# Kernel tuning notes

Measured on AMD Instinct MI355X. Metric: run time of the kernel, lower is better.

## Reference

```python
import jax, jax.numpy as jnp
import numpy as np

# NOTE: the original source omits the definitions of QSVT, quantum_lcu_block,
# QuantumSumBlock and KANLayer. We reconstruct the standard math these blocks
# implement in quantum-KAN papers/repos:
#   QSVT(x)            -> vector of Chebyshev polynomials T_1..T_D of the
#                         (squashed) input, the polynomial basis QSVT realizes.
#   quantum_lcu_block  -> linear combination of unitaries: weighted sum of the
#                         QSVT vector normalized by the LCU l1 weight norm.
#   QuantumSumBlock    -> learnable interference sum: mean_k sin(alpha_k * v).
#   KANLayer           -> Chebyshev-KAN layer: spline term (Chebyshev basis
#                         contracted with coeffs) + SiLU base branch + bias.
# Everything is fully vectorized over (B, F) instead of the original per-scalar
# Python loops.

B, F, DEG, C, KBASIS = 16384, 512, 8, 10, 8


def _cheb(x, K):
    """Chebyshev features T_1..T_K of x in (-1, 1): shape x.shape + (K,)."""
    t = jnp.arccos(jnp.clip(x, -1.0, 1.0))
    k = jnp.arange(1, K + 1, dtype=x.dtype)
    return jnp.cos(t[..., None] * k)


def setup_inputs() -> dict:
    key = jax.random.key(0)
    ks = jax.random.split(key, 6)
    return {
        "X": jax.random.normal(ks[0], (B, F), dtype=jnp.float32),
        # nn.Parameter(torch.rand(num_features, degree))
        "lcu_weights": jax.random.uniform(ks[1], (F, DEG), dtype=jnp.float32),
        # one QuantumSumBlock(degree) per feature -> (F, DEG) phases
        "sum_alpha": jax.random.normal(ks[2], (F, DEG), dtype=jnp.float32),
        # KANLayer params
        "kan_coeff": jax.random.normal(ks[3], (C, F, KBASIS), dtype=jnp.float32) * 0.1,
        "kan_base": jax.random.normal(ks[4], (C, F), dtype=jnp.float32) * 0.1,
        "kan_bias": jnp.zeros((C,), dtype=jnp.float32),
    }


def reference(X, lcu_weights, sum_alpha, kan_coeff, kan_base, kan_bias):
    # squash inputs into the open interval (-1, 1) for the Chebyshev/QSVT basis
    x = 0.99 * jnp.tanh(X)                                   # (B, F)
    # QSVT polynomial feature vector per scalar, batched: (B, F, DEG)
    qsvt = _cheb(x, lcu_weights.shape[1])
    # LCU block: weighted combination normalized by l1 norm of weights -> (B, F)
    lcu = jnp.einsum('bfd,fd->bf', qsvt, lcu_weights) / (
        jnp.sum(jnp.abs(lcu_weights), axis=-1) + 1e-8)
    # Quantum sum block: learnable sinusoidal interference sum -> (B, F)
    summed = jnp.mean(jnp.sin(lcu[..., None] * sum_alpha), axis=-1)
    # Chebyshev-KAN layer
    s = 0.99 * jnp.tanh(summed)
    phi = _cheb(s, kan_coeff.shape[2])                       # (B, F, KBASIS)
    logits = (jnp.einsum('bfk,cfk->bc', phi, kan_coeff)
              + jax.nn.silu(summed) @ kan_base.T
              + kan_bias)                                    # (B, C)
    return logits
```

## Files before the change

### kernel.cpp

```cpp
#include <hip/hip_runtime.h>
#include <hip/hip_bf16.h>

#define BATCH 16384
#define NF    512
#define DEG   8
#define NC    10
#define KB    8

#define RB    16
#define PITCH (NF + 4)
#define NT    256

#define CBN (NC * NF * KB)
#define BBN (NC * NF)

#define INV2PI 0.15915494309189535f
#define LOG2E  1.4426950408889634f

typedef __attribute__((ext_vector_type(2))) float v2f;
typedef __attribute__((ext_vector_type(8))) short bfrag;
typedef __attribute__((ext_vector_type(4))) float f32x4;

union frag_u { bfrag s; unsigned u[4]; };

__device__ unsigned short g_pk[CBN + BBN];

__device__ __forceinline__ v2f v2fma(v2f a, v2f b, v2f c) {
    return __builtin_elementwise_fma(a, b, c);
}
__device__ __forceinline__ v2f v2exp2(v2f a) {
    v2f r; r.x = __builtin_amdgcn_exp2f(a.x); r.y = __builtin_amdgcn_exp2f(a.y);
    return r;
}
__device__ __forceinline__ v2f v2rcp(v2f x) {
    v2f r; r.x = __builtin_amdgcn_rcpf(x.x); r.y = __builtin_amdgcn_rcpf(x.y);
    return r;
}
__device__ __forceinline__ v2f v2sin2pi(v2f x) {
    v2f r; r.x = __builtin_amdgcn_sinf(x.x); r.y = __builtin_amdgcn_sinf(x.y);
    return r;
}
__device__ __forceinline__ v2f v2tanh99(v2f x) {
    v2f e = v2exp2(x * (2.0f * LOG2E));
    v2f r = v2rcp(e + 1.0f);
    return v2fma(r, (v2f)(-1.98f), (v2f)(0.99f));
}
__device__ __forceinline__ v2f v2silu(v2f v) {
    v2f e = v2exp2(v * (-LOG2E));
    v2f r = v2rcp(e + 1.0f);
    return v * r;
}
__device__ __forceinline__ unsigned cvtpk2(float lo, float hi) {
    __hip_bfloat162 h = __float22bfloat162_rn(float2{lo, hi});
    unsigned u;
    __builtin_memcpy(&u, &h, sizeof(u));
    return u;
}

__global__ __launch_bounds__(256) void prep_kernel(
    const float* __restrict__ coeff, const float* __restrict__ base)
{
    const int i = blockIdx.x * 256 + threadIdx.x;
    if (i < CBN)
        g_pk[i] = (unsigned short)((__builtin_bit_cast(unsigned, coeff[i]) + 0x8000u) >> 16);
    else if (i < CBN + BBN)
        g_pk[i] = (unsigned short)((__builtin_bit_cast(unsigned, base[i - CBN]) + 0x8000u) >> 16);
}

__global__ __launch_bounds__(NT, 4) void qkan_kernel(
    const float* __restrict__ X,
    const float* __restrict__ lcu_w,
    const float* __restrict__ alpha,
    const float* __restrict__ bias,
    float* __restrict__ out)
{
    __shared__ float s_mem[RB * PITCH];
    __shared__ float s_red[4 * RB * 16];

    const int t    = threadIdx.x;
    const int row0 = blockIdx.x * RB;

    {
        const int fA = t * 2;

        float wa[2][DEG], aa[2][DEG], den[2];
#pragma unroll
        for (int i = 0; i < 2; ++i) {
            const float4 w0 = *(const float4*)(lcu_w + (fA + i) * DEG);
            const float4 w1 = *(const float4*)(lcu_w + (fA + i) * DEG + 4);
            const float4 a0 = *(const float4*)(alpha + (fA + i) * DEG);
            const float4 a1 = *(const float4*)(alpha + (fA + i) * DEG + 4);
            wa[i][0]=w0.x; wa[i][1]=w0.y; wa[i][2]=w0.z; wa[i][3]=w0.w;
            wa[i][4]=w1.x; wa[i][5]=w1.y; wa[i][6]=w1.z; wa[i][7]=w1.w;
            aa[i][0]=a0.x; aa[i][1]=a0.y; aa[i][2]=a0.z; aa[i][3]=a0.w;
            aa[i][4]=a1.x; aa[i][5]=a1.y; aa[i][6]=a1.z; aa[i][7]=a1.w;
            float d = 1e-8f;
#pragma unroll
            for (int k = 0; k < DEG; ++k) d += fabsf(wa[i][k]);
            den[i] = d;
        }
        v2f W[DEG], A2[DEG];
#pragma unroll
        for (int d = 0; d < DEG; ++d) {
            W[d]  = (v2f){wa[0][d], wa[1][d]};
            A2[d] = (v2f){aa[0][d] * INV2PI, aa[1][d] * INV2PI};
        }
        const v2f rden = (v2f){__builtin_amdgcn_rcpf(den[0]),
                               __builtin_amdgcn_rcpf(den[1])};

#pragma unroll 4
        for (int r = 0; r < RB; ++r) {
            const v2f xv = *(const v2f*)(X + (row0 + r) * NF + fA);
            const v2f x  = v2tanh99(xv);
            const v2f x2 = x + x;
            v2f tkm1 = (v2f){1.0f, 1.0f}, tk = x, num = (v2f){0.0f, 0.0f};
#pragma unroll
            for (int d = 0; d < DEG; ++d) {
                num = v2fma(W[d], tk, num);
                v2f tn = v2fma(x2, tk, -tkm1);
                tkm1 = tk; tk = tn;
            }
            const v2f lcu = num * rden;
            v2f ss = (v2f){0.0f, 0.0f};
#pragma unroll
            for (int d = 0; d < DEG; ++d)
                ss += v2sin2pi(lcu * A2[d]);
            *(v2f*)(&s_mem[r * PITCH + fA]) = ss * 0.125f;
        }
    }
    __syncthreads();

    const int lane = t & 63;
    const int wave = __builtin_amdgcn_readfirstlane(t >> 6);
    const int n    = lane & 15;
    const int q    = lane >> 4;
    const int ncl  = (n < NC) ? n : (NC - 1);
    const int fw   = wave * 128;

    const unsigned short* cb = g_pk;
    const unsigned short* bb = g_pk + CBN;
    const unsigned short* cbase = cb + (ncl * NF + fw) * KB;

    f32x4 acc0 = {0.f, 0.f, 0.f, 0.f};
    f32x4 acc1 = {0.f, 0.f, 0.f, 0.f};

#pragma unroll 4
    for (int kp = 0; kp < 16; ++kp) {
        const bfrag b0 = *(const bfrag*)(cbase + (kp * 8 + q) * KB);
        const bfrag b1 = *(const bfrag*)(cbase + (kp * 8 + 4 + q) * KB);

        const float sA = s_mem[n * PITCH + fw + kp * 8 + q];
        const float sB = s_mem[n * PITCH + fw + kp * 8 + 4 + q];
        const v2f s  = v2tanh99((v2f){sA, sB});
        const v2f s2 = s + s;
        v2f T[KB];
        {
            v2f tkm1 = (v2f){1.0f, 1.0f}, tk = s;
#pragma unroll
            for (int k = 0; k < KB; ++k) {
                T[k] = tk;
                v2f tn = v2fma(s2, tk, -tkm1);
                tkm1 = tk; tk = tn;
            }
        }
        frag_u fa0, fa1;
#pragma unroll
        for (int i = 0; i < 4; ++i) {
            fa0.u[i] = cvtpk2(T[2 * i].x, T[2 * i + 1].x);
            fa1.u[i] = cvtpk2(T[2 * i].y, T[2 * i + 1].y);
        }
        acc0 = __builtin_amdgcn_mfma_f32_16x16x32_bf16(fa0.s, b0, acc0, 0, 0, 0);
        acc1 = __builtin_amdgcn_mfma_f32_16x16x32_bf16(fa1.s, b1, acc1, 0, 0, 0);
    }

#pragma unroll
    for (int kt2 = 0; kt2 < 4; ++kt2) {
        const bfrag b = *(const bfrag*)(bb + ncl * NF + fw + kt2 * 32 + q * 8);
        const int off = n * PITCH + fw + kt2 * 32 + q * 8;
        const float4 v0 = *(const float4*)(&s_mem[off]);
        const float4 v1 = *(const float4*)(&s_mem[off + 4]);
        v2f vv[4] = {{v0.x, v0.y}, {v0.z, v0.w}, {v1.x, v1.y}, {v1.z, v1.w}};
        frag_u fa;
#pragma unroll
        for (int g = 0; g < 4; ++g) {
            const v2f sl = v2silu(vv[g]);
            fa.u[g] = cvtpk2(sl.x, sl.y);
        }
        if (kt2 & 1)
            acc1 = __builtin_amdgcn_mfma_f32_16x16x32_bf16(fa.s, b, acc1, 0, 0, 0);
        else
            acc0 = __builtin_amdgcn_mfma_f32_16x16x32_bf16(fa.s, b, acc0, 0, 0, 0);
    }

    const f32x4 acc = acc0 + acc1;
#pragma unroll
    for (int i = 0; i < 4; ++i)
        s_red[(wave * RB + q * 4 + i) * 16 + n] = acc[i];
    __syncthreads();

    if (t < RB * NC) {
        const int r = t / NC;
        const int c = t - r * NC;
        float v = bias[c];
#pragma unroll
        for (int w = 0; w < 4; ++w)
            v += s_red[(w * RB + r) * 16 + c];
        out[(row0 + r) * NC + c] = v;
    }
}

extern "C" void kernel_launch(void* const* d_in, const int* in_sizes, int n_in,
                              void* d_out, int out_size, void* d_ws, size_t ws_size,
                              hipStream_t stream) {
    const float* X      = (const float*)d_in[0];
    const float* lcu_w  = (const float*)d_in[1];
    const float* alpha  = (const float*)d_in[2];
    const float* coeff  = (const float*)d_in[3];
    const float* base   = (const float*)d_in[4];
    const float* bias   = (const float*)d_in[5];
    float* out = (float*)d_out;
    (void)d_ws; (void)ws_size;

    prep_kernel<<<(CBN + BBN + 255) / 256, 256, 0, stream>>>(coeff, base);
    qkan_kernel<<<BATCH / RB, NT, 0, stream>>>(X, lcu_w, alpha, bias, out);
}
```

Before: 100.0 us.

## Fold bf16 weight prep into main kernel and double rows per block

Removes the separate prep kernel that packed the KAN coefficients and base weights to bf16. The main kernel now reads fp32 weights and converts them in registers. Each block now handles 32 rows instead of 16, so every converted B fragment feeds two MFMAs, one per 16-row slab. Shared memory switches from a padded pitch to an XOR swizzle, and the reduction buffer reuses the feature buffer. This saves a launch and amortizes the weight loads, at the cost of twice the fp32 weight traffic per fragment, lower occupancy (launch bounds 2) and half as many blocks.

Result: no change. 101.1 us (+1.1%).

```diff
diff --git a/kernel.cpp b/kernel.cpp
--- a/kernel.cpp
+++ b/kernel.cpp
@@ -7,12 +7,8 @@
 #define NC    10
 #define KB    8
 
-#define RB    16
-#define PITCH (NF + 4)
+#define RB    32
 #define NT    256
-
-#define CBN (NC * NF * KB)
-#define BBN (NC * NF)
 
 #define INV2PI 0.15915494309189535f
 #define LOG2E  1.4426950408889634f
@@ -22,8 +18,6 @@
 typedef __attribute__((ext_vector_type(4))) float f32x4;
 
 union frag_u { bfrag s; unsigned u[4]; };
-
-__device__ unsigned short g_pk[CBN + BBN];
 
 __device__ __forceinline__ v2f v2fma(v2f a, v2f b, v2f c) {
     return __builtin_elementwise_fma(a, b, c);
@@ -56,26 +50,29 @@
     __builtin_memcpy(&u, &h, sizeof(u));
     return u;
 }
-
-__global__ __launch_bounds__(256) void prep_kernel(
-    const float* __restrict__ coeff, const float* __restrict__ base)
-{
-    const int i = blockIdx.x * 256 + threadIdx.x;
-    if (i < CBN)
-        g_pk[i] = (unsigned short)((__builtin_bit_cast(unsigned, coeff[i]) + 0x8000u) >> 16);
-    else if (i < CBN + BBN)
-        g_pk[i] = (unsigned short)((__builtin_bit_cast(unsigned, base[i - CBN]) + 0x8000u) >> 16);
-}
-
-__global__ __launch_bounds__(NT, 4) void qkan_kernel(
+__device__ __forceinline__ bfrag pack8(float4 a, float4 b) {
+    frag_u f;
+    f.u[0] = cvtpk2(a.x, a.y);
+    f.u[1] = cvtpk2(a.z, a.w);
+    f.u[2] = cvtpk2(b.x, b.y);
+    f.u[3] = cvtpk2(b.z, b.w);
+    return f.s;
+}
+
+__device__ __forceinline__ int swz(int row, int col) {
+    return row * NF + (col ^ ((row & 7) << 2));
+}
+
+__global__ __launch_bounds__(NT, 2) void qkan_kernel(
     const float* __restrict__ X,
     const float* __restrict__ lcu_w,
     const float* __restrict__ alpha,
+    const float* __restrict__ coeff,
+    const float* __restrict__ base,
     const float* __restrict__ bias,
     float* __restrict__ out)
 {
-    __shared__ float s_mem[RB * PITCH];
-    __shared__ float s_red[4 * RB * 16];
+    __shared__ float s_mem[RB * NF];
 
     const int t    = threadIdx.x;
     const int row0 = blockIdx.x * RB;
@@ -125,7 +122,7 @@
 #pragma unroll
             for (int d = 0; d < DEG; ++d)
                 ss += v2sin2pi(lcu * A2[d]);
-            *(v2f*)(&s_mem[r * PITCH + fA]) = ss * 0.125f;
+            *(v2f*)(&s_mem[swz(r, fA)]) = ss * 0.125f;
         }
     }
     __syncthreads();
@@ -137,70 +134,100 @@
     const int ncl  = (n < NC) ? n : (NC - 1);
     const int fw   = wave * 128;
 
-    const unsigned short* cb = g_pk;
-    const unsigned short* bb = g_pk + CBN;
-    const unsigned short* cbase = cb + (ncl * NF + fw) * KB;
-
-    f32x4 acc0 = {0.f, 0.f, 0.f, 0.f};
-    f32x4 acc1 = {0.f, 0.f, 0.f, 0.f};
+    const float* cbF = coeff + (ncl * NF + fw) * KB;
+    const float* bbF = base + ncl * NF + fw;
+
+    f32x4 acc00 = {0.f,0.f,0.f,0.f}, acc01 = {0.f,0.f,0.f,0.f};
+    f32x4 acc10 = {0.f,0.f,0.f,0.f}, acc11 = {0.f,0.f,0.f,0.f};
 
 #pragma unroll 4
     for (int kp = 0; kp < 16; ++kp) {
-        const bfrag b0 = *(const bfrag*)(cbase + (kp * 8 + q) * KB);
-        const bfrag b1 = *(const bfrag*)(cbase + (kp * 8 + 4 + q) * KB);
-
-        const float sA = s_mem[n * PITCH + fw + kp * 8 + q];
-        const float sB = s_mem[n * PITCH + fw + kp * 8 + 4 + q];
-        const v2f s  = v2tanh99((v2f){sA, sB});
-        const v2f s2 = s + s;
-        v2f T[KB];
-        {
-            v2f tkm1 = (v2f){1.0f, 1.0f}, tk = s;
-#pragma unroll
-            for (int k = 0; k < KB; ++k) {
-                T[k] = tk;
-                v2f tn = v2fma(s2, tk, -tkm1);
-                tkm1 = tk; tk = tn;
-            }
-        }
-        frag_u fa0, fa1;
+        const float* c0p = cbF + (kp * 8 + q) * KB;
+        const float* c1p = cbF + (kp * 8 + 4 + q) * KB;
+        const bfrag b0 = pack8(*(const float4*)(c0p), *(const float4*)(c0p + 4));
+        const bfrag b1 = pack8(*(const float4*)(c1p), *(const float4*)(c1p + 4));
+
+#pragma unroll
+        for (int rs = 0; rs < 2; ++rs) {
+            const int row = n + rs * 16;
+            const float sA = s_mem[swz(row, fw + kp * 8 + q)];
+            const float sB = s_mem[swz(row, fw + kp * 8 + 4 + q)];
+            const v2f s  = v2tanh99((v2f){sA, sB});
+            const v2f s2 = s + s;
+            v2f T[KB];
+            {
+                v2f tkm1 = (v2f){1.0f, 1.0f}, tk = s;
+#pragma unroll
+                for (int k = 0; k < KB; ++k) {
+                    T[k] = tk;
+                    v2f tn = v2fma(s2, tk, -tkm1);
+                    tkm1 = tk; tk = tn;
+                }
+            }
+            frag_u fa0, fa1;
+#pragma unroll
+            for (int i = 0; i < 4; ++i) {
+                fa0.u[i] = cvtpk2(T[2 * i].x, T[2 * i + 1].x);
+                fa1.u[i] = cvtpk2(T[2 * i].y, T[2 * i + 1].y);
+            }
+            if (rs == 0) {
+                acc00 = __builtin_amdgcn_mfma_f32_16x16x32_bf16(fa0.s, b0, acc00, 0, 0, 0);
+                acc01 = __builtin_amdgcn_mfma_f32_16x16x32_bf16(fa1.s, b1, acc01, 0, 0, 0);
+            } else {
+                acc10 = __builtin_amdgcn_mfma_f32_16x16x32_bf16(fa0.s, b0, acc10, 0, 0, 0);
+                acc11 = __builtin_amdgcn_mfma_f32_16x16x32_bf16(fa1.s, b1, acc11, 0, 0, 0);
+            }
+        }
+    }
+
+#pragma unroll
+    for (int kt2 = 0; kt2 < 4; ++kt2) {
+        const float* bp = bbF + kt2 * 32 + q * 8;
+        const bfrag b = pack8(*(const float4*)(bp), *(const float4*)(bp + 4));
+
+#pragma unroll
+        for (int rs = 0; rs < 2; ++rs) {
+            const int row = n + rs * 16;
+            const int col = fw + kt2 * 32 + q * 8;
+            const float4 v0 = *(const float4*)(&s_mem[swz(row, col)]);
+            const float4 v1 = *(const float4*)(&s_mem[swz(row, col + 4)]);
+            v2f vv[4] = {{v0.x, v0.y}, {v0.z, v0.w}, {v1.x, v1.y}, {v1.z, v1.w}};
+            frag_u fa;
+#pragma unroll
+            for (int g = 0; g < 4; ++g) {
+                const v2f sl = v2silu(vv[g]);
+                fa.u[g] = cvtpk2(sl.x, sl.y);
+            }
+            if (rs == 0) {
+                if (kt2 & 1)
+                    acc01 = __builtin_amdgcn_mfma_f32_16x16x32_bf16(fa.s, b, acc01, 0, 0, 0);
+                else
+                    acc00 = __builtin_amdgcn_mfma_f32_16x16x32_bf16(fa.s, b, acc00, 0, 0, 0);
+            } else {
+                if (kt2 & 1)
+                    acc11 = __builtin_amdgcn_mfma_f32_16x16x32_bf16(fa.s, b, acc11, 0, 0, 0);
+                else
+                    acc10 = __builtin_amdgcn_mfma_f32_16x16x32_bf16(fa.s, b, acc10, 0, 0, 0);
+            }
+        }
+    }
+
+    __syncthreads();
+    float* s_red = s_mem;
+    {
+        const f32x4 accA = acc00 + acc01;
+        const f32x4 accB = acc10 + acc11;
 #pragma unroll
         for (int i = 0; i < 4; ++i) {
-            fa0.u[i] = cvtpk2(T[2 * i].x, T[2 * i + 1].x);
-            fa1.u[i] = cvtpk2(T[2 * i].y, T[2 * i + 1].y);
-        }
-        acc0 = __builtin_amdgcn_mfma_f32_16x16x32_bf16(fa0.s, b0, acc0, 0, 0, 0);
-        acc1 = __builtin_amdgcn_mfma_f32_16x16x32_bf16(fa1.s, b1, acc1, 0, 0, 0);
-    }
-
-#pragma unroll
-    for (int kt2 = 0; kt2 < 4; ++kt2) {
-        const bfrag b = *(const bfrag*)(bb + ncl * NF + fw + kt2 * 32 + q * 8);
-        const int off = n * PITCH + fw + kt2 * 32 + q * 8;
-        const float4 v0 = *(const float4*)(&s_mem[off]);
-        const float4 v1 = *(const float4*)(&s_mem[off + 4]);
-        v2f vv[4] = {{v0.x, v0.y}, {v0.z, v0.w}, {v1.x, v1.y}, {v1.z, v1.w}};
-        frag_u fa;
-#pragma unroll
-        for (int g = 0; g < 4; ++g) {
-            const v2f sl = v2silu(vv[g]);
-            fa.u[g] = cvtpk2(sl.x, sl.y);
-        }
-        if (kt2 & 1)
-            acc1 = __builtin_amdgcn_mfma_f32_16x16x32_bf16(fa.s, b, acc1, 0, 0, 0);
-        else
-            acc0 = __builtin_amdgcn_mfma_f32_16x16x32_bf16(fa.s, b, acc0, 0, 0, 0);
-    }
-
-    const f32x4 acc = acc0 + acc1;
-#pragma unroll
-    for (int i = 0; i < 4; ++i)
-        s_red[(wave * RB + q * 4 + i) * 16 + n] = acc[i];
+            s_red[(wave * RB + q * 4 + i) * 16 + n] = accA[i];
+            s_red[(wave * RB + 16 + q * 4 + i) * 16 + n] = accB[i];
+        }
+    }
     __syncthreads();
 
-    if (t < RB * NC) {
-        const int r = t / NC;
-        const int c = t - r * NC;
+    for (int idx = t; idx < RB * NC; idx += NT) {
+        const int r = idx / NC;
+        const int c = idx - r * NC;
         float v = bias[c];
 #pragma unroll
         for (int w = 0; w < 4; ++w)
@@ -221,6 +248,5 @@
     float* out = (float*)d_out;
     (void)d_ws; (void)ws_size;
 
-    prep_kernel<<<(CBN + BBN + 255) / 256, 256, 0, stream>>>(coeff, base);
-    qkan_kernel<<<BATCH / RB, NT, 0, stream>>>(X, lcu_w, alpha, bias, out);
-}
+    qkan_kernel<<<BATCH / RB, NT, 0, stream>>>(X, lcu_w, alpha, coeff, base, bias, out);
+}
```
